# Kernel tuning notes

Hardware: AMD Instinct MI355X
Metric: run time of the kernel (lower is better)

Reference implementation:

```python
import jax, jax.numpy as jnp
import numpy as np

IN_DIM, OUT_DIM = 256, 64
ALPHA = 0.2  # leaky relu negative slope
NEG_INF = -1e30


def setup_inputs() -> dict:
    key = jax.random.key(0)
    k1, k2, k3, k4 = jax.random.split(key, 4)
    B, N = 8, 2048
    h = jax.random.normal(k1, (B, N, IN_DIM), dtype=jnp.float32)
    adj = jax.random.randint(k2, (B, N, N), 0, 2, dtype=jnp.int32)
    # ensure no fully-isolated node (avoids softmax over all -inf)
    idx = jnp.arange(N)
    adj = adj.at[:, idx, idx].set(1)
    # params: fc.weight [out,in] -> store transposed [in,out]; attn_fc.weight [1, 2*out] -> [2*out]
    W = jax.random.normal(k3, (IN_DIM, OUT_DIM), dtype=jnp.float32) / np.sqrt(IN_DIM)
    a = jax.random.normal(k4, (2 * OUT_DIM,), dtype=jnp.float32) / np.sqrt(2 * OUT_DIM)
    return {"h": h, "adj": adj, "W": W, "a": a}


def reference(h, adj, W, a):
    # Wh: [B,N,D]
    Wh = jnp.einsum("bni,io->bno", h, W)
    D = Wh.shape[-1]
    # concat-based additive attention decomposed: e[b,i,j] = lrelu(a1.Wh_i + a2.Wh_j)
    a1, a2 = a[:D], a[D:]
    s1 = Wh @ a1  # [B,N] contribution of row node i
    s2 = Wh @ a2  # [B,N] contribution of col node j
    e = jax.nn.leaky_relu(s1[:, :, None] + s2[:, None, :], negative_slope=ALPHA)  # [B,N,N]
    e = jnp.where(adj == 0, NEG_INF, e)
    attn = jax.nn.softmax(e, axis=-1)
    # dropout is identity in eval mode
    return jnp.einsum("bij,bjd->bid", attn, Wh)
```

## Files before the change

### kernel.cpp

```cpp
#include <hip/hip_runtime.h>
#include <math.h>

#define NB 8
#define NN 2048
#define IN_DIM 256
#define OUT_DIM 64
#define ALPHA 0.2f
#define JSPLIT 4

typedef __attribute__((ext_vector_type(8))) short bf16x8;
typedef __attribute__((ext_vector_type(4))) float f32x4;

__device__ __forceinline__ unsigned short f2bf(float x) {
    union { float f; unsigned u; } v; v.f = x;
    unsigned r = v.u + 0x7FFF + ((v.u >> 16) & 1);
    return (unsigned short)(r >> 16);
}

#define WT_STRIDE 264
__global__ __launch_bounds__(256) void wh_kernel(const float* __restrict__ h,
                                                 const float* __restrict__ W,
                                                 const float* __restrict__ a,
                                                 unsigned short* __restrict__ Whbt,
                                                 float* __restrict__ s1,
                                                 float* __restrict__ s2) {
    __shared__ unsigned short Wt[OUT_DIM * WT_STRIDE];
    const int t = threadIdx.x;

    #pragma unroll 8
    for (int rep = 0; rep < 64; ++rep) {
        const int id = rep * 256 + t;
        const int k = id >> 6, n = id & 63;
        Wt[n * WT_STRIDE + k] = f2bf(W[id]);
    }
    __syncthreads();

    const int lane = t & 63, wv = t >> 6;
    const int m = lane & 15, quad = lane >> 4;
    const long gr0 = (long)(blockIdx.x * 4 + wv) * 16;

    f32x4 acc[4];
    #pragma unroll
    for (int nt = 0; nt < 4; ++nt) acc[nt] = (f32x4){0.f, 0.f, 0.f, 0.f};

    #pragma unroll
    for (int ks = 0; ks < 8; ++ks) {
        const int k0 = ks * 32;
        const float* hp = h + (gr0 + m) * IN_DIM + k0 + quad * 8;
        const float4 ha = *(const float4*)hp;
        const float4 hb = *(const float4*)(hp + 4);
        bf16x8 af;
        af[0] = (short)f2bf(ha.x); af[1] = (short)f2bf(ha.y);
        af[2] = (short)f2bf(ha.z); af[3] = (short)f2bf(ha.w);
        af[4] = (short)f2bf(hb.x); af[5] = (short)f2bf(hb.y);
        af[6] = (short)f2bf(hb.z); af[7] = (short)f2bf(hb.w);
        #pragma unroll
        for (int nt = 0; nt < 4; ++nt) {
            const bf16x8 bf_ = *(const bf16x8*)(const void*)
                &Wt[(nt * 16 + m) * WT_STRIDE + k0 + quad * 8];
            acc[nt] = __builtin_amdgcn_mfma_f32_16x16x32_bf16(af, bf_, acc[nt], 0, 0, 0);
        }
    }

    const int b  = (int)(gr0 >> 11);
    const int ib = (int)(gr0 & 2047);

    #pragma unroll
    for (int nt = 0; nt < 4; ++nt) {
        ushort4 w4;
        w4.x = f2bf(acc[nt][0]); w4.y = f2bf(acc[nt][1]);
        w4.z = f2bf(acc[nt][2]); w4.w = f2bf(acc[nt][3]);
        *(ushort4*)&Whbt[((long)(b * OUT_DIM + nt * 16 + m) << 11) + ib + quad * 4] = w4;
    }

    float a1v[4], a2v[4];
    #pragma unroll
    for (int nt = 0; nt < 4; ++nt) {
        a1v[nt] = a[nt * 16 + m];
        a2v[nt] = a[OUT_DIM + nt * 16 + m];
    }
    #pragma unroll
    for (int reg = 0; reg < 4; ++reg) {
        float p1 = 0.f, p2 = 0.f;
        #pragma unroll
        for (int nt = 0; nt < 4; ++nt) {
            p1 += acc[nt][reg] * a1v[nt];
            p2 += acc[nt][reg] * a2v[nt];
        }
        #pragma unroll
        for (int off = 1; off < 16; off <<= 1) {
            p1 += __shfl_xor(p1, off, 64);
            p2 += __shfl_xor(p2, off, 64);
        }
        if (m == 0) {
            s1[gr0 + quad * 4 + reg] = p1;
            s2[gr0 + quad * 4 + reg] = p2;
        }
    }
}

#define PSTR 40
__global__ __launch_bounds__(256) void attn_kernel(const int* __restrict__ adj,
                                                   const unsigned short* __restrict__ Whbt,
                                                   const float* __restrict__ s1,
                                                   const float* __restrict__ s2,
                                                   float* __restrict__ part,
                                                   float* __restrict__ lpart) {
    __shared__ unsigned short p_all[4][16 * PSTR];

    const int t = threadIdx.x, lane = t & 63, wv = t >> 6;
    unsigned short* p_lds = &p_all[wv][0];

    const int bid = blockIdx.x;
    const int js  = bid & (JSPLIT - 1);
    const int itg = (bid >> 2) & 31;
    const int b   = bid >> 7;
    const int i0  = itg * 64 + wv * 16;
    const int jlo = js * (NN / JSPLIT);

    const int rhalf = lane >> 5, jj = lane & 31;
    const int m = lane & 15, quad = lane >> 4;

    float s1r[8];
    #pragma unroll
    for (int k = 0; k < 8; ++k) s1r[k] = s1[b * NN + i0 + rhalf + 2 * k];

    f32x4 acc[4];
    #pragma unroll
    for (int nt = 0; nt < 4; ++nt) acc[nt] = (f32x4){0.f, 0.f, 0.f, 0.f};
    float lacc[8] = {0.f, 0.f, 0.f, 0.f, 0.f, 0.f, 0.f, 0.f};

    const int* adjp = adj + (long)b * NN * NN + (long)(i0 + rhalf) * NN + jlo + jj;
    const unsigned short* wbase = Whbt + ((long)(b * OUT_DIM) << 11) + jlo;
    const float* s2p = s2 + b * NN + jlo + jj;

    int av[8];
    #pragma unroll
    for (int k = 0; k < 8; ++k)
        av[k] = __builtin_nontemporal_load(adjp + (long)(2 * k) * NN);

    for (int ks = 0; ks < 16; ++ks) {
        const int j0 = ks * 32;

        bf16x8 bfr[4];
        #pragma unroll
        for (int nt = 0; nt < 4; ++nt)
            bfr[nt] = *(const bf16x8*)(const void*)
                &wbase[((long)(nt * 16 + m) << 11) + j0 + quad * 8];

        const float s2v = s2p[j0];
        #pragma unroll
        for (int k = 0; k < 8; ++k) {
            float e = s1r[k] + s2v;
            e = e > 0.f ? e : ALPHA * e;
            const float p = (av[k] != 0) ? __expf(e) : 0.f;
            lacc[k] += p;
            p_lds[(rhalf + 2 * k) * PSTR + jj] = f2bf(p);
        }

        const int jn = (ks < 15) ? j0 + 32 : j0;
        #pragma unroll
        for (int k = 0; k < 8; ++k)
            av[k] = __builtin_nontemporal_load(adjp + (long)(2 * k) * NN + jn);

        asm volatile("s_waitcnt lgkmcnt(0)" ::: "memory");

        const bf16x8 af = *(const bf16x8*)(const void*)&p_lds[m * PSTR + quad * 8];
        #pragma unroll
        for (int nt = 0; nt < 4; ++nt)
            acc[nt] = __builtin_amdgcn_mfma_f32_16x16x32_bf16(af, bfr[nt], acc[nt], 0, 0, 0);
    }

    #pragma unroll
    for (int k = 0; k < 8; ++k) {
        float s = lacc[k];
        #pragma unroll
        for (int off = 1; off < 32; off <<= 1) s += __shfl_xor(s, off, 64);
        if (jj == 0)
            lpart[js * (NB * NN) + b * NN + i0 + rhalf + 2 * k] = s;
    }

    float* pp = part + (long)js * ((long)NB * NN * OUT_DIM)
                     + ((long)(b * NN + i0) << 6);
    #pragma unroll
    for (int nt = 0; nt < 4; ++nt)
        #pragma unroll
        for (int reg = 0; reg < 4; ++reg)
            pp[(quad * 4 + reg) * OUT_DIM + nt * 16 + m] = acc[nt][reg];
}

__global__ __launch_bounds__(256) void finalize_kernel(const float* __restrict__ part,
                                                       const float* __restrict__ lpart,
                                                       float* __restrict__ out) {
    const int idx = blockIdx.x * 256 + threadIdx.x;
    const int row = idx >> 4;
    float l = 0.f;
    #pragma unroll
    for (int s = 0; s < JSPLIT; ++s) l += lpart[s * (NB * NN) + row];
    float4 v = make_float4(0.f, 0.f, 0.f, 0.f);
    const float4* p4 = (const float4*)part;
    #pragma unroll
    for (int s = 0; s < JSPLIT; ++s) {
        const float4 p = p4[(long)s * ((long)NB * NN * OUT_DIM / 4) + idx];
        v.x += p.x; v.y += p.y; v.z += p.z; v.w += p.w;
    }
    const float inv = 1.f / l;
    v.x *= inv; v.y *= inv; v.z *= inv; v.w *= inv;
    ((float4*)out)[idx] = v;
}

extern "C" void kernel_launch(void* const* d_in, const int* in_sizes, int n_in,
                              void* d_out, int out_size, void* d_ws, size_t ws_size,
                              hipStream_t stream) {
    const float* h   = (const float*)d_in[0];
    const int*   adj = (const int*)d_in[1];
    const float* W   = (const float*)d_in[2];
    const float* a   = (const float*)d_in[3];
    float* out = (float*)d_out;

    float* s1    = (float*)d_ws;
    float* s2    = s1 + NB * NN;
    float* lpart = s2 + NB * NN;
    float* part  = lpart + JSPLIT * NB * NN;
    unsigned short* Whbt = (unsigned short*)(part + (long)JSPLIT * NB * NN * OUT_DIM);

    wh_kernel<<<NB * NN / 64, 256, 0, stream>>>(h, W, a, Whbt, s1, s2);
    attn_kernel<<<NB * (NN / 64) * JSPLIT, 256, 0, stream>>>(adj, Whbt, s1, s2, part, lpart);
    finalize_kernel<<<NB * NN * OUT_DIM / 4 / 256, 256, 0, stream>>>(part, lpart, out);
}
```

Baseline: 232.1 us.

## Compute attention probabilities directly in MFMA A-fragment layout, drop LDS staging

The attention kernel now assigns each lane the exact row and 8-column slice it needs as the MFMA A operand, loads adjacency and s2 as 128-bit vectors, and builds the bf16 fragment in registers with packed converts. This removes the LDS round-trip and its waitcnt barrier plus the per-element 32-bit adjacency loads. JSPLIT goes from 4 to 8 for more blocks, which doubles the partial-result traffic the finalize kernel must reduce. The wh kernel also uses the packed bf16 convert instruction.

```diff
diff --git a/kernel.cpp b/kernel.cpp
--- a/kernel.cpp
+++ b/kernel.cpp
@@ -6,15 +6,22 @@
 #define IN_DIM 256
 #define OUT_DIM 64
 #define ALPHA 0.2f
-#define JSPLIT 4
+#define JSPLIT 8
 
 typedef __attribute__((ext_vector_type(8))) short bf16x8;
 typedef __attribute__((ext_vector_type(4))) float f32x4;
+typedef __attribute__((ext_vector_type(4))) int i32x4;
 
 __device__ __forceinline__ unsigned short f2bf(float x) {
     union { float f; unsigned u; } v; v.f = x;
     unsigned r = v.u + 0x7FFF + ((v.u >> 16) & 1);
     return (unsigned short)(r >> 16);
+}
+
+__device__ __forceinline__ unsigned cvt_pk_bf16(float lo, float hi) {
+    unsigned r;
+    asm("v_cvt_pk_bf16_f32 %0, %1, %2" : "=v"(r) : "v"(lo), "v"(hi));
+    return r;
 }
 
 #define WT_STRIDE 264
@@ -49,16 +56,16 @@
         const float* hp = h + (gr0 + m) * IN_DIM + k0 + quad * 8;
         const float4 ha = *(const float4*)hp;
         const float4 hb = *(const float4*)(hp + 4);
-        bf16x8 af;
-        af[0] = (short)f2bf(ha.x); af[1] = (short)f2bf(ha.y);
-        af[2] = (short)f2bf(ha.z); af[3] = (short)f2bf(ha.w);
-        af[4] = (short)f2bf(hb.x); af[5] = (short)f2bf(hb.y);
-        af[6] = (short)f2bf(hb.z); af[7] = (short)f2bf(hb.w);
+        union { bf16x8 v; unsigned u32[4]; } af;
+        af.u32[0] = cvt_pk_bf16(ha.x, ha.y);
+        af.u32[1] = cvt_pk_bf16(ha.z, ha.w);
+        af.u32[2] = cvt_pk_bf16(hb.x, hb.y);
+        af.u32[3] = cvt_pk_bf16(hb.z, hb.w);
         #pragma unroll
         for (int nt = 0; nt < 4; ++nt) {
             const bf16x8 bf_ = *(const bf16x8*)(const void*)
                 &Wt[(nt * 16 + m) * WT_STRIDE + k0 + quad * 8];
-            acc[nt] = __builtin_amdgcn_mfma_f32_16x16x32_bf16(af, bf_, acc[nt], 0, 0, 0);
+            acc[nt] = __builtin_amdgcn_mfma_f32_16x16x32_bf16(af.v, bf_, acc[nt], 0, 0, 0);
         }
     }
 
@@ -99,86 +106,89 @@
     }
 }
 
-#define PSTR 40
 __global__ __launch_bounds__(256) void attn_kernel(const int* __restrict__ adj,
                                                    const unsigned short* __restrict__ Whbt,
                                                    const float* __restrict__ s1,
                                                    const float* __restrict__ s2,
                                                    float* __restrict__ part,
                                                    float* __restrict__ lpart) {
-    __shared__ unsigned short p_all[4][16 * PSTR];
-
     const int t = threadIdx.x, lane = t & 63, wv = t >> 6;
-    unsigned short* p_lds = &p_all[wv][0];
 
     const int bid = blockIdx.x;
     const int js  = bid & (JSPLIT - 1);
-    const int itg = (bid >> 2) & 31;
-    const int b   = bid >> 7;
+    const int itg = (bid >> 3) & 31;
+    const int b   = bid >> 8;
     const int i0  = itg * 64 + wv * 16;
     const int jlo = js * (NN / JSPLIT);
 
-    const int rhalf = lane >> 5, jj = lane & 31;
     const int m = lane & 15, quad = lane >> 4;
 
-    float s1r[8];
-    #pragma unroll
-    for (int k = 0; k < 8; ++k) s1r[k] = s1[b * NN + i0 + rhalf + 2 * k];
+    const float s1v = s1[b * NN + i0 + m];
 
     f32x4 acc[4];
     #pragma unroll
     for (int nt = 0; nt < 4; ++nt) acc[nt] = (f32x4){0.f, 0.f, 0.f, 0.f};
-    float lacc[8] = {0.f, 0.f, 0.f, 0.f, 0.f, 0.f, 0.f, 0.f};
-
-    const int* adjp = adj + (long)b * NN * NN + (long)(i0 + rhalf) * NN + jlo + jj;
-    const unsigned short* wbase = Whbt + ((long)(b * OUT_DIM) << 11) + jlo;
-    const float* s2p = s2 + b * NN + jlo + jj;
-
-    int av[8];
-    #pragma unroll
-    for (int k = 0; k < 8; ++k)
-        av[k] = __builtin_nontemporal_load(adjp + (long)(2 * k) * NN);
-
-    for (int ks = 0; ks < 16; ++ks) {
+    float lacc = 0.f;
+
+    const int* adjp = adj + (long)b * NN * NN + (long)(i0 + m) * NN + jlo + quad * 8;
+    const float* s2p = s2 + b * NN + jlo + quad * 8;
+    const unsigned short* wbase = Whbt + ((long)(b * OUT_DIM) << 11) + jlo + quad * 8;
+
+    i32x4 av0 = __builtin_nontemporal_load((const i32x4*)adjp);
+    i32x4 av1 = __builtin_nontemporal_load((const i32x4*)(adjp + 4));
+    f32x4 sv0 = *(const f32x4*)s2p;
+    f32x4 sv1 = *(const f32x4*)(s2p + 4);
+
+    const int NSTEP = NN / JSPLIT / 32;
+    for (int ks = 0; ks < NSTEP; ++ks) {
         const int j0 = ks * 32;
 
         bf16x8 bfr[4];
         #pragma unroll
         for (int nt = 0; nt < 4; ++nt)
             bfr[nt] = *(const bf16x8*)(const void*)
-                &wbase[((long)(nt * 16 + m) << 11) + j0 + quad * 8];
-
-        const float s2v = s2p[j0];
-        #pragma unroll
-        for (int k = 0; k < 8; ++k) {
-            float e = s1r[k] + s2v;
-            e = e > 0.f ? e : ALPHA * e;
-            const float p = (av[k] != 0) ? __expf(e) : 0.f;
-            lacc[k] += p;
-            p_lds[(rhalf + 2 * k) * PSTR + jj] = f2bf(p);
-        }
-
-        const int jn = (ks < 15) ? j0 + 32 : j0;
-        #pragma unroll
-        for (int k = 0; k < 8; ++k)
-            av[k] = __builtin_nontemporal_load(adjp + (long)(2 * k) * NN + jn);
-
-        asm volatile("s_waitcnt lgkmcnt(0)" ::: "memory");
-
-        const bf16x8 af = *(const bf16x8*)(const void*)&p_lds[m * PSTR + quad * 8];
+                &wbase[((long)(nt * 16 + m) << 11) + j0];
+
+        const i32x4 a0 = av0, a1 = av1;
+        const f32x4 t0 = sv0, t1 = sv1;
+        const int jn = (ks + 1 < NSTEP) ? j0 + 32 : j0;
+        av0 = __builtin_nontemporal_load((const i32x4*)(adjp + jn));
+        av1 = __builtin_nontemporal_load((const i32x4*)(adjp + jn + 4));
+        sv0 = *(const f32x4*)(s2p + jn);
+        sv1 = *(const f32x4*)(s2p + jn + 4);
+
+        float p[8];
+        #pragma unroll
+        for (int u = 0; u < 4; ++u) {
+            float e = s1v + t0[u];
+            e = fmaxf(e, ALPHA * e);
+            const float ex = __expf(e);
+            p[u] = (a0[u] != 0) ? ex : 0.f;
+        }
+        #pragma unroll
+        for (int u = 0; u < 4; ++u) {
+            float e = s1v + t1[u];
+            e = fmaxf(e, ALPHA * e);
+            const float ex = __expf(e);
+            p[4 + u] = (a1[u] != 0) ? ex : 0.f;
+        }
+        lacc += ((p[0] + p[1]) + (p[2] + p[3])) + ((p[4] + p[5]) + (p[6] + p[7]));
+
+        union { bf16x8 v; unsigned u32[4]; } af;
+        af.u32[0] = cvt_pk_bf16(p[0], p[1]);
+        af.u32[1] = cvt_pk_bf16(p[2], p[3]);
+        af.u32[2] = cvt_pk_bf16(p[4], p[5]);
+        af.u32[3] = cvt_pk_bf16(p[6], p[7]);
+
         #pragma unroll
         for (int nt = 0; nt < 4; ++nt)
-            acc[nt] = __builtin_amdgcn_mfma_f32_16x16x32_bf16(af, bfr[nt], acc[nt], 0, 0, 0);
-    }
-
-    #pragma unroll
-    for (int k = 0; k < 8; ++k) {
-        float s = lacc[k];
-        #pragma unroll
-        for (int off = 1; off < 32; off <<= 1) s += __shfl_xor(s, off, 64);
-        if (jj == 0)
-            lpart[js * (NB * NN) + b * NN + i0 + rhalf + 2 * k] = s;
-    }
+            acc[nt] = __builtin_amdgcn_mfma_f32_16x16x32_bf16(af.v, bfr[nt], acc[nt], 0, 0, 0);
+    }
+
+    lacc += __shfl_xor(lacc, 16, 64);
+    lacc += __shfl_xor(lacc, 32, 64);
+    if (quad == 0)
+        lpart[js * (NB * NN) + b * NN + i0 + m] = lacc;
 
     float* pp = part + (long)js * ((long)NB * NN * OUT_DIM)
                      + ((long)(b * NN + i0) << 6);
```

Result: slower. 244.0 us (+5.1%).
